# Performance work log

Hardware: AMD Instinct MI355X
Metric: run time of the kernel (lower is better)

## Reference

```python
import jax, jax.numpy as jnp
import numpy as np

EMBED = 512
HEADS = 8
DIM_HEAD = 64
SCALE = DIM_HEAD ** -0.5


def setup_inputs() -> dict:
    key = jax.random.key(0)
    k1, k2, k3 = jax.random.split(key, 3)
    x = jax.random.normal(k1, (1, EMBED, 64, 64), dtype=jnp.float32)
    # nn.Linear(embed, 3*embed) weight [out, in] -> store transposed [in, out] for x @ W
    W_qkv = jax.random.normal(k2, (EMBED, 3 * EMBED), dtype=jnp.float32) * (EMBED ** -0.5)
    b_qkv = jax.random.normal(k3, (3 * EMBED,), dtype=jnp.float32) * 0.01
    return {"x": x, "W_qkv": W_qkv, "b_qkv": b_qkv}


def reference(x, W_qkv, b_qkv):
    B, E, h, w = x.shape
    N = h * w
    # [B, E, H, W] -> [B, N, E]
    xs = x.reshape(B, E, N).transpose(0, 2, 1)
    qkv = xs @ W_qkv + b_qkv                      # [B, N, 3E]
    q, k, v = jnp.split(qkv, 3, axis=-1)          # each [B, N, E]

    def heads(t):
        return t.reshape(B, N, HEADS, DIM_HEAD).transpose(0, 2, 1, 3)  # [B, H, N, dh]

    q, k, v = heads(q), heads(k), heads(v)
    # raw (non-softmax) attention scores, materialized as in the original
    attn = jnp.einsum('bhqd,bhkd->bhqk', q, k) * SCALE  # [B, H, N, N]
    coarse_attn = attn.sum(axis=-2)                     # sum over queries -> [B, H, N]
    output = jnp.einsum('bhqk,bhkd->bhqd', attn, v)     # [B, H, N, dh]
    return coarse_attn, output
```

## Files before the change

kernel.cpp:

```cpp
#include <hip/hip_runtime.h>


#define N_TOK 4096
#define EMBED 512
#define J3    1536
#define HEADS 8
#define DH    64
#define SCALE 0.125f

typedef float  floatx4  __attribute__((ext_vector_type(4)));
typedef short  shortx8  __attribute__((ext_vector_type(8)));
typedef unsigned short ushortx4 __attribute__((ext_vector_type(4)));
typedef unsigned short ushortx2 __attribute__((ext_vector_type(2)));
typedef unsigned int u32;

__device__ inline unsigned short f2bf(float f) {
    union { float f; u32 u; } x; x.f = f;
    u32 r = x.u + 0x7fffu + ((x.u >> 16) & 1u);
    return (unsigned short)(r >> 16);
}
__device__ inline float bf2f(unsigned short u) {
    union { u32 u; float f; } x; x.u = ((u32)u) << 16; return x.f;
}
__device__ static inline void async_copy16(void* lds, const void* g) {
    auto* gp = (const __attribute__((address_space(1))) u32*)g;
    auto* lp = (__attribute__((address_space(3))) u32*)lds;
    __builtin_amdgcn_global_load_lds(gp, lp, 16, 0, 0);
}

__global__ __launch_bounds__(256) void tr_cvt(const float* __restrict__ x,
                                              const float* __restrict__ W,
                                              unsigned short* __restrict__ xT,
                                              unsigned short* __restrict__ WT) {
    const float* src; unsigned short* dst; int C, bx = blockIdx.x;
    if (bx < 64) { src = x; dst = xT; C = N_TOK; }
    else         { src = W; dst = WT; C = J3; bx -= 64; }
    __shared__ float T[64][65];
    const int c0 = bx * 64, r0 = blockIdx.y * 64;
    const int t = threadIdx.x;
    #pragma unroll
    for (int k = 0; k < 16; ++k) {
        int i = t + 256 * k; int r = i >> 6, c = i & 63;
        T[r][c] = src[(size_t)(r0 + r) * C + c0 + c];
    }
    __syncthreads();
    #pragma unroll
    for (int k = 0; k < 4; ++k) {
        int i = t + 256 * k; int cr = i >> 4, cc4 = (i & 15) * 4;
        ushortx4 o = { f2bf(T[cc4 + 0][cr]), f2bf(T[cc4 + 1][cr]),
                       f2bf(T[cc4 + 2][cr]), f2bf(T[cc4 + 3][cr]) };
        *(ushortx4*)&dst[(size_t)(c0 + cr) * 512 + r0 + cc4] = o;
    }
}

__global__ __launch_bounds__(256) void qkv_mfma(const unsigned short* __restrict__ xT,
                                                const unsigned short* __restrict__ WT,
                                                const float* __restrict__ bias,
                                                unsigned short* __restrict__ qkv) {
    __shared__ __align__(16) short As[128 * 32];
    __shared__ __align__(16) short Bs[128 * 32];
    const int j0 = blockIdx.x * 128, n0 = blockIdx.y * 128;
    const int t = threadIdx.x, lane = t & 63, w = t >> 6;
    const int wm = w & 1, wn = w >> 1;
    const int quad = lane >> 4, mrow = lane & 15;
    floatx4 acc[4][4] = {};
    for (int e0 = 0; e0 < 512; e0 += 32) {
        __syncthreads();
        #pragma unroll
        for (int s = 0; s < 2; ++s) {
            int i = t + 256 * s;
            int row = i >> 2, q = i & 3;
            char* abase = (char*)As + (size_t)w * 1024 + (size_t)s * 4096;
            char* bbase = (char*)Bs + (size_t)w * 1024 + (size_t)s * 4096;
            async_copy16(abase, xT + (size_t)(n0 + row) * 512 + e0 + q * 8);
            async_copy16(bbase, WT + (size_t)(j0 + row) * 512 + e0 + q * 8);
        }
        __syncthreads();
        shortx8 a[4], b[4];
        #pragma unroll
        for (int mi = 0; mi < 4; ++mi)
            a[mi] = *(const shortx8*)&As[(wm * 64 + mi * 16 + mrow) * 32 + quad * 8];
        #pragma unroll
        for (int ni = 0; ni < 4; ++ni)
            b[ni] = *(const shortx8*)&Bs[(wn * 64 + ni * 16 + mrow) * 32 + quad * 8];
        #pragma unroll
        for (int mi = 0; mi < 4; ++mi)
            #pragma unroll
            for (int ni = 0; ni < 4; ++ni)
                acc[mi][ni] = __builtin_amdgcn_mfma_f32_16x16x32_bf16(a[mi], b[ni], acc[mi][ni], 0, 0, 0);
    }
    const int col = lane & 15, qr = lane >> 4;
    #pragma unroll
    for (int ni = 0; ni < 4; ++ni) {
        int j = j0 + wn * 64 + ni * 16 + col;
        float bj = bias[j];
        #pragma unroll
        for (int mi = 0; mi < 4; ++mi)
            #pragma unroll
            for (int r = 0; r < 4; ++r) {
                int n = n0 + wm * 64 + mi * 16 + qr * 4 + r;
                qkv[(size_t)n * J3 + j] = f2bf(acc[mi][ni][r] + bj);
            }
    }
}

__global__ __launch_bounds__(256) void kv_partial(const unsigned short* __restrict__ qkv,
                                                  float* __restrict__ Mp, float* __restrict__ qsp) {
    const int h = blockIdx.x, ch = blockIdx.y;
    const int n0 = ch * 64;
    __shared__ __align__(16) float Ks[64][68];
    __shared__ __align__(16) float Vs[64][68];
    __shared__ float qred[256];
    const int t = threadIdx.x;
    #pragma unroll
    for (int k = 0; k < 2; ++k) {
        int i = t + 256 * k; int row = i >> 3, c8 = (i & 7) * 8;
        shortx8 k8 = *(const shortx8*)(qkv + (size_t)(n0 + row) * J3 + EMBED + h * DH + c8);
        shortx8 v8 = *(const shortx8*)(qkv + (size_t)(n0 + row) * J3 + 2 * EMBED + h * DH + c8);
        #pragma unroll
        for (int j = 0; j < 8; ++j) {
            Ks[row][c8 + j] = bf2f((unsigned short)k8[j]);
            Vs[row][c8 + j] = bf2f((unsigned short)v8[j]);
        }
    }
    {
        int d = t & 63, q0 = (t >> 6) * 16;
        float qa = 0.f;
        for (int n = q0; n < q0 + 16; ++n)
            qa += bf2f(qkv[(size_t)(n0 + n) * J3 + h * DH + d]);
        qred[t] = qa;
    }
    __syncthreads();
    const int tx = t & 15, ty = t >> 4;
    float acc[4][4] = {};
    for (int n = 0; n < 64; ++n) {
        floatx4 kf = *(const floatx4*)&Ks[n][ty * 4];
        floatx4 vf = *(const floatx4*)&Vs[n][tx * 4];
        #pragma unroll
        for (int i = 0; i < 4; ++i)
            #pragma unroll
            for (int j = 0; j < 4; ++j)
                acc[i][j] += kf[i] * vf[j];
    }
    float* mp = Mp + ((size_t)h * 64 + ch) * 4096;
    #pragma unroll
    for (int i = 0; i < 4; ++i) {
        floatx4 v = { acc[i][0], acc[i][1], acc[i][2], acc[i][3] };
        *(floatx4*)&mp[(ty * 4 + i) * 64 + tx * 4] = v;
    }
    if (t < 64)
        qsp[((size_t)h * 64 + ch) * 64 + t] = qred[t] + qred[t + 64] + qred[t + 128] + qred[t + 192];
}

__global__ __launch_bounds__(256) void reduce_md(const float* __restrict__ Mp,
                                                 const float* __restrict__ qsp,
                                                 unsigned short* __restrict__ Mt,
                                                 float* __restrict__ qsum) {
    const int h = blockIdx.x, part = blockIdx.y;
    const int t = threadIdx.x;
    __shared__ float Msh[16][68];
    const int i0 = part * 1024 + t * 4;
    floatx4 s = {0.f, 0.f, 0.f, 0.f};
    #pragma unroll 4
    for (int c = 0; c < 64; ++c)
        s += *(const floatx4*)&Mp[((size_t)h * 64 + c) * 4096 + i0];
    const int dpl = t >> 4, d0 = (t & 15) * 4;
    *(floatx4*)&Msh[dpl][d0] = s;
    __syncthreads();
    {
        int d = t >> 2, dpl0 = (t & 3) * 4;
        ushortx4 o = { f2bf(Msh[dpl0 + 0][d]), f2bf(Msh[dpl0 + 1][d]),
                       f2bf(Msh[dpl0 + 2][d]), f2bf(Msh[dpl0 + 3][d]) };
        *(ushortx4*)&Mt[(size_t)h * 4096 + d * 64 + part * 16 + dpl0] = o;
    }
    if (part == 0 && t < 64) {
        float q = 0.f;
        for (int c = 0; c < 64; ++c) q += qsp[((size_t)h * 64 + c) * 64 + t];
        qsum[h * DH + t] = q;
    }
}

__global__ __launch_bounds__(64) void out_kernel(const unsigned short* __restrict__ qkv,
                                                 const unsigned short* __restrict__ Mt,
                                                 const float* __restrict__ qsum,
                                                 float* __restrict__ out) {
    const int h = blockIdx.x, n0 = blockIdx.y * 64;
    const int lane = threadIdx.x;
    const int quad = lane >> 4, mrow = lane & 15;
    floatx4 acc[4][4] = {};
    #pragma unroll
    for (int ks = 0; ks < 2; ++ks) {
        shortx8 a[4], b[4];
        #pragma unroll
        for (int mi = 0; mi < 4; ++mi)
            a[mi] = *(const shortx8*)(qkv + (size_t)(n0 + mi * 16 + mrow) * J3 + h * DH + ks * 32 + quad * 8);
        #pragma unroll
        for (int ni = 0; ni < 4; ++ni)
            b[ni] = *(const shortx8*)(Mt + (size_t)h * 4096 + (ni * 16 + mrow) * 64 + ks * 32 + quad * 8);
        #pragma unroll
        for (int mi = 0; mi < 4; ++mi)
            #pragma unroll
            for (int ni = 0; ni < 4; ++ni)
                acc[mi][ni] = __builtin_amdgcn_mfma_f32_16x16x32_bf16(a[mi], b[ni], acc[mi][ni], 0, 0, 0);
    }
    float* op = out + HEADS * N_TOK + (size_t)h * N_TOK * DH;
    #pragma unroll
    for (int mi = 0; mi < 4; ++mi)
        #pragma unroll
        for (int r = 0; r < 4; ++r) {
            int n = n0 + mi * 16 + quad * 4 + r;
            #pragma unroll
            for (int ni = 0; ni < 4; ++ni)
                op[(size_t)n * DH + ni * 16 + mrow] = acc[mi][ni][r] * SCALE;
        }
    float ca = 0.f;
    #pragma unroll
    for (int g = 0; g < 8; ++g) {
        shortx8 kk = *(const shortx8*)(qkv + (size_t)(n0 + lane) * J3 + EMBED + h * DH + g * 8);
        #pragma unroll
        for (int j = 0; j < 8; ++j)
            ca += bf2f((unsigned short)kk[j]) * qsum[h * DH + g * 8 + j];
    }
    out[h * N_TOK + n0 + lane] = ca * SCALE;
}

extern "C" void kernel_launch(void* const* d_in, const int* in_sizes, int n_in,
                              void* d_out, int out_size, void* d_ws, size_t ws_size,
                              hipStream_t stream) {
    const float* x = (const float*)d_in[0];
    const float* W = (const float*)d_in[1];
    const float* b = (const float*)d_in[2];
    float* out = (float*)d_out;

    unsigned short* xT   = (unsigned short*)d_ws;
    unsigned short* WT   = xT + (size_t)N_TOK * EMBED;
    unsigned short* qkvb = WT + (size_t)J3 * EMBED;
    unsigned short* Mt   = qkvb + (size_t)N_TOK * J3;
    float* Mp   = (float*)(Mt + (size_t)HEADS * DH * DH);
    float* qsp  = Mp + (size_t)HEADS * 64 * 4096;
    float* qsum = qsp + (size_t)HEADS * 64 * 64;

    tr_cvt<<<dim3(88, 8), 256, 0, stream>>>(x, W, xT, WT);
    qkv_mfma<<<dim3(12, 32), 256, 0, stream>>>(xT, WT, b, qkvb);
    kv_partial<<<dim3(8, 64), 256, 0, stream>>>(qkvb, Mp, qsp);
    reduce_md<<<dim3(8, 4), 256, 0, stream>>>(Mp, qsp, Mt, qsum);
    out_kernel<<<dim3(8, 64), 64, 0, stream>>>(qkvb, Mt, qsum, out);
}
```

Baseline: 107.4 us.

## Fold K^T V into weights and compute output via single GEMM from x

Reworks the pipeline algebraically. Q is no longer materialized: the per-head K^T V matrix is folded into the Q weight slice, giving a 640x512 combined matrix. Output and coarse attention are then produced by one GEMM over x. The query column sum is taken from x column sums times W_q plus the bias. K/V projection and the per-chunk K^T V product are fused into one MFMA kernel, so the full qkv buffer is never written. This adds a fold kernel, atomics and a memset, and rounds the folded weights to bf16, which may change accuracy.

```diff
diff --git a/kernel.cpp b/kernel.cpp
--- a/kernel.cpp
+++ b/kernel.cpp
@@ -11,15 +11,15 @@
 typedef float  floatx4  __attribute__((ext_vector_type(4)));
 typedef short  shortx8  __attribute__((ext_vector_type(8)));
 typedef unsigned short ushortx4 __attribute__((ext_vector_type(4)));
-typedef unsigned short ushortx2 __attribute__((ext_vector_type(2)));
 typedef unsigned int u32;
-
-__device__ inline unsigned short f2bf(float f) {
+typedef unsigned short ushort;
+
+__device__ inline ushort f2bf(float f) {
     union { float f; u32 u; } x; x.f = f;
     u32 r = x.u + 0x7fffu + ((x.u >> 16) & 1u);
-    return (unsigned short)(r >> 16);
-}
-__device__ inline float bf2f(unsigned short u) {
+    return (ushort)(r >> 16);
+}
+__device__ inline float bf2f(ushort u) {
     union { u32 u; float f; } x; x.u = ((u32)u) << 16; return x.f;
 }
 __device__ static inline void async_copy16(void* lds, const void* g) {
@@ -28,22 +28,50 @@
     __builtin_amdgcn_global_load_lds(gp, lp, 16, 0, 0);
 }
 
-__global__ __launch_bounds__(256) void tr_cvt(const float* __restrict__ x,
-                                              const float* __restrict__ W,
-                                              unsigned short* __restrict__ xT,
-                                              unsigned short* __restrict__ WT) {
-    const float* src; unsigned short* dst; int C, bx = blockIdx.x;
-    if (bx < 64) { src = x; dst = xT; C = N_TOK; }
-    else         { src = W; dst = WT; C = J3; bx -= 64; }
+__global__ __launch_bounds__(256) void prep(const float* __restrict__ x,
+                                            const float* __restrict__ W,
+                                            ushort* __restrict__ xT,
+                                            ushort* __restrict__ WT,
+                                            ushort* __restrict__ Wb,
+                                            float* __restrict__ xsum) {
+    const int t = threadIdx.x;
+    int bx = blockIdx.x;
+    if (bx >= 88) {
+        if (blockIdx.y != 0) return;
+        const int e0 = (bx - 88) * 32;
+        #pragma unroll
+        for (int k = 0; k < 2; ++k) {
+            int i = t + 256 * k; int row = e0 + (i >> 4), c = (i & 15) * 32;
+            #pragma unroll
+            for (int v = 0; v < 8; ++v) {
+                floatx4 f = *(const floatx4*)(W + (size_t)row * J3 + c + v * 4);
+                ushortx4 o = { f2bf(f[0]), f2bf(f[1]), f2bf(f[2]), f2bf(f[3]) };
+                *(ushortx4*)(Wb + (size_t)row * 512 + c + v * 4) = o;
+            }
+        }
+        return;
+    }
+    const bool isx = bx < 64;
+    const float* src = isx ? x : W;
+    ushort* dst = isx ? xT : WT;
+    const int C = isx ? N_TOK : J3;
+    if (!isx) bx -= 64;
     __shared__ float T[64][65];
+    __shared__ float red[256];
     const int c0 = bx * 64, r0 = blockIdx.y * 64;
-    const int t = threadIdx.x;
     #pragma unroll
     for (int k = 0; k < 16; ++k) {
         int i = t + 256 * k; int r = i >> 6, c = i & 63;
         T[r][c] = src[(size_t)(r0 + r) * C + c0 + c];
     }
     __syncthreads();
+    if (isx) {
+        int row = t >> 2, seg = (t & 3) * 16;
+        float s = 0.f;
+        #pragma unroll
+        for (int cc = 0; cc < 16; ++cc) s += T[row][seg + cc];
+        red[t] = s;
+    }
     #pragma unroll
     for (int k = 0; k < 4; ++k) {
         int i = t + 256 * k; int cr = i >> 4, cc4 = (i & 15) * 4;
@@ -51,114 +79,109 @@
                        f2bf(T[cc4 + 2][cr]), f2bf(T[cc4 + 3][cr]) };
         *(ushortx4*)&dst[(size_t)(c0 + cr) * 512 + r0 + cc4] = o;
     }
-}
-
-__global__ __launch_bounds__(256) void qkv_mfma(const unsigned short* __restrict__ xT,
-                                                const unsigned short* __restrict__ WT,
-                                                const float* __restrict__ bias,
-                                                unsigned short* __restrict__ qkv) {
-    __shared__ __align__(16) short As[128 * 32];
-    __shared__ __align__(16) short Bs[128 * 32];
-    const int j0 = blockIdx.x * 128, n0 = blockIdx.y * 128;
-    const int t = threadIdx.x, lane = t & 63, w = t >> 6;
-    const int wm = w & 1, wn = w >> 1;
-    const int quad = lane >> 4, mrow = lane & 15;
-    floatx4 acc[4][4] = {};
-    for (int e0 = 0; e0 < 512; e0 += 32) {
-        __syncthreads();
-        #pragma unroll
-        for (int s = 0; s < 2; ++s) {
-            int i = t + 256 * s;
-            int row = i >> 2, q = i & 3;
-            char* abase = (char*)As + (size_t)w * 1024 + (size_t)s * 4096;
-            char* bbase = (char*)Bs + (size_t)w * 1024 + (size_t)s * 4096;
-            async_copy16(abase, xT + (size_t)(n0 + row) * 512 + e0 + q * 8);
-            async_copy16(bbase, WT + (size_t)(j0 + row) * 512 + e0 + q * 8);
-        }
-        __syncthreads();
-        shortx8 a[4], b[4];
-        #pragma unroll
-        for (int mi = 0; mi < 4; ++mi)
-            a[mi] = *(const shortx8*)&As[(wm * 64 + mi * 16 + mrow) * 32 + quad * 8];
-        #pragma unroll
-        for (int ni = 0; ni < 4; ++ni)
-            b[ni] = *(const shortx8*)&Bs[(wn * 64 + ni * 16 + mrow) * 32 + quad * 8];
-        #pragma unroll
-        for (int mi = 0; mi < 4; ++mi)
-            #pragma unroll
-            for (int ni = 0; ni < 4; ++ni)
-                acc[mi][ni] = __builtin_amdgcn_mfma_f32_16x16x32_bf16(a[mi], b[ni], acc[mi][ni], 0, 0, 0);
-    }
-    const int col = lane & 15, qr = lane >> 4;
-    #pragma unroll
-    for (int ni = 0; ni < 4; ++ni) {
-        int j = j0 + wn * 64 + ni * 16 + col;
-        float bj = bias[j];
-        #pragma unroll
-        for (int mi = 0; mi < 4; ++mi)
-            #pragma unroll
-            for (int r = 0; r < 4; ++r) {
-                int n = n0 + wm * 64 + mi * 16 + qr * 4 + r;
-                qkv[(size_t)n * J3 + j] = f2bf(acc[mi][ni][r] + bj);
-            }
-    }
-}
-
-__global__ __launch_bounds__(256) void kv_partial(const unsigned short* __restrict__ qkv,
-                                                  float* __restrict__ Mp, float* __restrict__ qsp) {
+    if (isx) {
+        __syncthreads();
+        if ((t & 3) == 0)
+            atomicAdd(&xsum[r0 + (t >> 2)], red[t] + red[t + 1] + red[t + 2] + red[t + 3]);
+    }
+}
+
+__global__ __launch_bounds__(256) void kv_mfma(const ushort* __restrict__ xT,
+                                               const ushort* __restrict__ WT,
+                                               const float* __restrict__ bias,
+                                               float* __restrict__ Mp) {
     const int h = blockIdx.x, ch = blockIdx.y;
     const int n0 = ch * 64;
-    __shared__ __align__(16) float Ks[64][68];
-    __shared__ __align__(16) float Vs[64][68];
-    __shared__ float qred[256];
-    const int t = threadIdx.x;
-    #pragma unroll
-    for (int k = 0; k < 2; ++k) {
-        int i = t + 256 * k; int row = i >> 3, c8 = (i & 7) * 8;
-        shortx8 k8 = *(const shortx8*)(qkv + (size_t)(n0 + row) * J3 + EMBED + h * DH + c8);
-        shortx8 v8 = *(const shortx8*)(qkv + (size_t)(n0 + row) * J3 + 2 * EMBED + h * DH + c8);
-        #pragma unroll
-        for (int j = 0; j < 8; ++j) {
-            Ks[row][c8 + j] = bf2f((unsigned short)k8[j]);
-            Vs[row][c8 + j] = bf2f((unsigned short)v8[j]);
-        }
+    __shared__ __align__(16) short As[64 * 32];
+    __shared__ __align__(16) short Bs[128 * 32];
+    __shared__ __align__(16) short Kt[64 * 72];
+    __shared__ __align__(16) short Vt[64 * 72];
+    const int t = threadIdx.x, lane = t & 63, w = t >> 6;
+    const int quad = lane >> 4, mrow = lane & 15;
+    floatx4 acc[4][2] = {};
+    for (int e0 = 0; e0 < 512; e0 += 32) {
+        __syncthreads();
+        {
+            int row = t >> 2, q = t & 3;
+            async_copy16((char*)As + (size_t)w * 1024,
+                         xT + (size_t)(n0 + row) * 512 + e0 + q * 8);
+        }
+        #pragma unroll
+        for (int s = 0; s < 2; ++s) {
+            int i = t + 256 * s; int row = i >> 2, q = i & 3;
+            int j = (row < 64) ? (512 + h * 64 + row) : (1024 + h * 64 + row - 64);
+            async_copy16((char*)Bs + (size_t)w * 1024 + (size_t)s * 4096,
+                         WT + (size_t)j * 512 + e0 + q * 8);
+        }
+        __syncthreads();
+        shortx8 a[4], b[2];
+        #pragma unroll
+        for (int mi = 0; mi < 4; ++mi)
+            a[mi] = *(const shortx8*)&As[(mi * 16 + mrow) * 32 + quad * 8];
+        #pragma unroll
+        for (int ni = 0; ni < 2; ++ni)
+            b[ni] = *(const shortx8*)&Bs[(w * 32 + ni * 16 + mrow) * 32 + quad * 8];
+        #pragma unroll
+        for (int mi = 0; mi < 4; ++mi)
+            #pragma unroll
+            for (int ni = 0; ni < 2; ++ni)
+                acc[mi][ni] = __builtin_amdgcn_mfma_f32_16x16x32_bf16(a[mi], b[ni], acc[mi][ni], 0, 0, 0);
     }
     {
-        int d = t & 63, q0 = (t >> 6) * 16;
-        float qa = 0.f;
-        for (int n = q0; n < q0 + 16; ++n)
-            qa += bf2f(qkv[(size_t)(n0 + n) * J3 + h * DH + d]);
-        qred[t] = qa;
+        short* dst = (w < 2) ? Kt : Vt;
+        const int dhb = (w & 1) * 32;
+        const int boff = (w < 2) ? 512 : 1024;
+        #pragma unroll
+        for (int ni = 0; ni < 2; ++ni) {
+            int dh = dhb + ni * 16 + (lane & 15);
+            float bj = bias[boff + h * 64 + dh];
+            #pragma unroll
+            for (int mi = 0; mi < 4; ++mi)
+                #pragma unroll
+                for (int r = 0; r < 4; ++r) {
+                    int tok = mi * 16 + quad * 4 + r;
+                    dst[dh * 72 + tok] = (short)f2bf(acc[mi][ni][r] + bj);
+                }
+        }
     }
     __syncthreads();
-    const int tx = t & 15, ty = t >> 4;
-    float acc[4][4] = {};
-    for (int n = 0; n < 64; ++n) {
-        floatx4 kf = *(const floatx4*)&Ks[n][ty * 4];
-        floatx4 vf = *(const floatx4*)&Vs[n][tx * 4];
-        #pragma unroll
-        for (int i = 0; i < 4; ++i)
-            #pragma unroll
-            for (int j = 0; j < 4; ++j)
-                acc[i][j] += kf[i] * vf[j];
+    const int dpb = (w & 1) * 32, db = (w >> 1) * 32;
+    floatx4 m[2][2] = {};
+    #pragma unroll
+    for (int kt = 0; kt < 2; ++kt) {
+        shortx8 ka[2], vb[2];
+        #pragma unroll
+        for (int fi = 0; fi < 2; ++fi)
+            ka[fi] = *(const shortx8*)&Kt[(dpb + fi * 16 + mrow) * 72 + kt * 32 + quad * 8];
+        #pragma unroll
+        for (int fj = 0; fj < 2; ++fj)
+            vb[fj] = *(const shortx8*)&Vt[(db + fj * 16 + mrow) * 72 + kt * 32 + quad * 8];
+        #pragma unroll
+        for (int fi = 0; fi < 2; ++fi)
+            #pragma unroll
+            for (int fj = 0; fj < 2; ++fj)
+                m[fi][fj] = __builtin_amdgcn_mfma_f32_16x16x32_bf16(ka[fi], vb[fj], m[fi][fj], 0, 0, 0);
     }
     float* mp = Mp + ((size_t)h * 64 + ch) * 4096;
     #pragma unroll
-    for (int i = 0; i < 4; ++i) {
-        floatx4 v = { acc[i][0], acc[i][1], acc[i][2], acc[i][3] };
-        *(floatx4*)&mp[(ty * 4 + i) * 64 + tx * 4] = v;
-    }
-    if (t < 64)
-        qsp[((size_t)h * 64 + ch) * 64 + t] = qred[t] + qred[t + 64] + qred[t + 128] + qred[t + 192];
-}
-
-__global__ __launch_bounds__(256) void reduce_md(const float* __restrict__ Mp,
-                                                 const float* __restrict__ qsp,
-                                                 unsigned short* __restrict__ Mt,
+    for (int fi = 0; fi < 2; ++fi)
+        #pragma unroll
+        for (int fj = 0; fj < 2; ++fj)
+            #pragma unroll
+            for (int r = 0; r < 4; ++r)
+                mp[(dpb + fi * 16 + quad * 4 + r) * 64 + db + fj * 16 + (lane & 15)] = m[fi][fj][r];
+}
+
+__global__ __launch_bounds__(256) void reduce_qm(const float* __restrict__ Mp,
+                                                 const ushort* __restrict__ WT,
+                                                 const float* __restrict__ bias,
+                                                 const float* __restrict__ xsum,
+                                                 ushort* __restrict__ Mt,
                                                  float* __restrict__ qsum) {
     const int h = blockIdx.x, part = blockIdx.y;
     const int t = threadIdx.x;
     __shared__ float Msh[16][68];
+    __shared__ float red[256];
     const int i0 = part * 1024 + t * 4;
     floatx4 s = {0.f, 0.f, 0.f, 0.f};
     #pragma unroll 4
@@ -173,55 +196,143 @@
                        f2bf(Msh[dpl0 + 2][d]), f2bf(Msh[dpl0 + 3][d]) };
         *(ushortx4*)&Mt[(size_t)h * 4096 + d * 64 + part * 16 + dpl0] = o;
     }
-    if (part == 0 && t < 64) {
-        float q = 0.f;
-        for (int c = 0; c < 64; ++c) q += qsp[((size_t)h * 64 + c) * 64 + t];
-        qsum[h * DH + t] = q;
-    }
-}
-
-__global__ __launch_bounds__(64) void out_kernel(const unsigned short* __restrict__ qkv,
-                                                 const unsigned short* __restrict__ Mt,
-                                                 const float* __restrict__ qsum,
-                                                 float* __restrict__ out) {
-    const int h = blockIdx.x, n0 = blockIdx.y * 64;
-    const int lane = threadIdx.x;
+    {
+        int row = t >> 4, seg = (t & 15) * 32;
+        int j = h * 64 + part * 16 + row;
+        float qa = 0.f;
+        #pragma unroll
+        for (int g = 0; g < 4; ++g) {
+            shortx8 wv = *(const shortx8*)(WT + (size_t)j * 512 + seg + g * 8);
+            #pragma unroll
+            for (int u = 0; u < 8; ++u)
+                qa += bf2f((ushort)wv[u]) * xsum[seg + g * 8 + u];
+        }
+        red[t] = qa;
+    }
+    __syncthreads();
+    if (t < 16) {
+        float tot = 0.f;
+        #pragma unroll
+        for (int g = 0; g < 16; ++g) tot += red[t * 16 + g];
+        int j = h * 64 + part * 16 + t;
+        qsum[j] = 4096.f * bias[j] + tot;
+    }
+}
+
+__global__ __launch_bounds__(256) void fold(const ushort* __restrict__ Wb,
+                                            const float* __restrict__ W,
+                                            const float* __restrict__ bias,
+                                            const ushort* __restrict__ Mt,
+                                            const float* __restrict__ qsum,
+                                            ushort* __restrict__ B2,
+                                            float* __restrict__ b2) {
+    const int h = blockIdx.x;
+    const int t = threadIdx.x, lane = t & 63, w = t >> 6;
+    const int quad = lane >> 4, mrow = lane & 15;
+    for (int pos = w; pos < 128; pos += 4) {
+        int mi = pos >> 5, nj = pos & 31;
+        floatx4 d4 = {};
+        #pragma unroll
+        for (int k = 0; k < 2; ++k) {
+            shortx8 a = *(const shortx8*)(Mt + (size_t)h * 4096 + (mi * 16 + mrow) * 64 + k * 32 + quad * 8);
+            shortx8 b = *(const shortx8*)(Wb + (size_t)(nj * 16 + mrow) * 512 + h * 64 + k * 32 + quad * 8);
+            d4 = __builtin_amdgcn_mfma_f32_16x16x32_bf16(a, b, d4, 0, 0, 0);
+        }
+        #pragma unroll
+        for (int r = 0; r < 4; ++r) {
+            int d = mi * 16 + quad * 4 + r, e = nj * 16 + (lane & 15);
+            B2[(size_t)(h * 64 + d) * 512 + e] = f2bf(d4[r]);
+        }
+    }
+    for (int e = t; e < 512; e += 256) {
+        const float* wr = W + (size_t)e * J3 + 512 + h * 64;
+        const float* qh = qsum + h * 64;
+        float s = 0.f;
+        #pragma unroll 8
+        for (int dp = 0; dp < 64; ++dp) s += wr[dp] * qh[dp];
+        B2[(size_t)(512 + h) * 512 + e] = f2bf(s);
+    }
+    {
+        shortx8 z = {};
+        for (int idx = t; idx < 960; idx += 256)
+            *(shortx8*)(B2 + (size_t)(520 + h * 15) * 512 + idx * 8) = z;
+    }
+    if (t < 64) {
+        float s = 0.f;
+        #pragma unroll 8
+        for (int dp = 0; dp < 64; ++dp)
+            s += bias[h * 64 + dp] * bf2f(Mt[(size_t)h * 4096 + t * 64 + dp]);
+        b2[h * 64 + t] = s;
+    } else if (t == 64) {
+        float s = 0.f;
+        for (int dp = 0; dp < 64; ++dp)
+            s += bias[512 + h * 64 + dp] * qsum[h * 64 + dp];
+        b2[512 + h] = s;
+    }
+    if (h == 0 && t >= 128 && t < 248) b2[520 + (t - 128)] = 0.f;
+}
+
+__global__ __launch_bounds__(256) void out_gemm(const ushort* __restrict__ xT,
+                                                const ushort* __restrict__ B2,
+                                                const float* __restrict__ b2,
+                                                float* __restrict__ out) {
+    __shared__ __align__(16) short As[128 * 32];
+    __shared__ __align__(16) short Bs[128 * 32];
+    const int j0 = blockIdx.x * 128, n0 = blockIdx.y * 128;
+    const int t = threadIdx.x, lane = t & 63, w = t >> 6;
+    const int wm = w & 1, wn = w >> 1;
     const int quad = lane >> 4, mrow = lane & 15;
     floatx4 acc[4][4] = {};
-    #pragma unroll
-    for (int ks = 0; ks < 2; ++ks) {
+    for (int e0 = 0; e0 < 512; e0 += 32) {
+        __syncthreads();
+        #pragma unroll
+        for (int s = 0; s < 2; ++s) {
+            int i = t + 256 * s; int row = i >> 2, q = i & 3;
+            async_copy16((char*)As + (size_t)w * 1024 + (size_t)s * 4096,
+                         xT + (size_t)(n0 + row) * 512 + e0 + q * 8);
+            async_copy16((char*)Bs + (size_t)w * 1024 + (size_t)s * 4096,
+                         B2 + (size_t)(j0 + row) * 512 + e0 + q * 8);
+        }
+        __syncthreads();
         shortx8 a[4], b[4];
         #pragma unroll
         for (int mi = 0; mi < 4; ++mi)
-            a[mi] = *(const shortx8*)(qkv + (size_t)(n0 + mi * 16 + mrow) * J3 + h * DH + ks * 32 + quad * 8);
+            a[mi] = *(const shortx8*)&As[(wm * 64 + mi * 16 + mrow) * 32 + quad * 8];
         #pragma unroll
         for (int ni = 0; ni < 4; ++ni)
-            b[ni] = *(const shortx8*)(Mt + (size_t)h * 4096 + (ni * 16 + mrow) * 64 + ks * 32 + quad * 8);
+            b[ni] = *(const shortx8*)&Bs[(wn * 64 + ni * 16 + mrow) * 32 + quad * 8];
         #pragma unroll
         for (int mi = 0; mi < 4; ++mi)
             #pragma unroll
             for (int ni = 0; ni < 4; ++ni)
                 acc[mi][ni] = __builtin_amdgcn_mfma_f32_16x16x32_bf16(a[mi], b[ni], acc[mi][ni], 0, 0, 0);
     }
-    float* op = out + HEADS * N_TOK + (size_t)h * N_TOK * DH;
-    #pragma unroll
-    for (int mi = 0; mi < 4; ++mi)
-        #pragma unroll
-        for (int r = 0; r < 4; ++r) {
-            int n = n0 + mi * 16 + quad * 4 + r;
-            #pragma unroll
-            for (int ni = 0; ni < 4; ++ni)
-                op[(size_t)n * DH + ni * 16 + mrow] = acc[mi][ni][r] * SCALE;
-        }
-    float ca = 0.f;
-    #pragma unroll
-    for (int g = 0; g < 8; ++g) {
-        shortx8 kk = *(const shortx8*)(qkv + (size_t)(n0 + lane) * J3 + EMBED + h * DH + g * 8);
-        #pragma unroll
-        for (int j = 0; j < 8; ++j)
-            ca += bf2f((unsigned short)kk[j]) * qsum[h * DH + g * 8 + j];
-    }
-    out[h * N_TOK + n0 + lane] = ca * SCALE;
+    const int col = lane & 15, qr = lane >> 4;
+    #pragma unroll
+    for (int ni = 0; ni < 4; ++ni) {
+        int j = j0 + wn * 64 + ni * 16 + col;
+        float bj = b2[j];
+        if (j < 512) {
+            int hh = j >> 6, d = j & 63;
+            float* op = out + HEADS * N_TOK + (size_t)hh * N_TOK * DH + d;
+            #pragma unroll
+            for (int mi = 0; mi < 4; ++mi)
+                #pragma unroll
+                for (int r = 0; r < 4; ++r) {
+                    int n = n0 + wm * 64 + mi * 16 + qr * 4 + r;
+                    op[(size_t)n * DH] = SCALE * (acc[mi][ni][r] + bj);
+                }
+        } else if (j < 520) {
+            int hh = j - 512;
+            #pragma unroll
+            for (int mi = 0; mi < 4; ++mi)
+                #pragma unroll
+                for (int r = 0; r < 4; ++r) {
+                    int n = n0 + wm * 64 + mi * 16 + qr * 4 + r;
+                    out[hh * N_TOK + n] = SCALE * (acc[mi][ni][r] + bj);
+                }
+        }
+    }
 }
 
 extern "C" void kernel_launch(void* const* d_in, const int* in_sizes, int n_in,
@@ -232,17 +343,20 @@
     const float* b = (const float*)d_in[2];
     float* out = (float*)d_out;
 
-    unsigned short* xT   = (unsigned short*)d_ws;
-    unsigned short* WT   = xT + (size_t)N_TOK * EMBED;
-    unsigned short* qkvb = WT + (size_t)J3 * EMBED;
-    unsigned short* Mt   = qkvb + (size_t)N_TOK * J3;
-    float* Mp   = (float*)(Mt + (size_t)HEADS * DH * DH);
-    float* qsp  = Mp + (size_t)HEADS * 64 * 4096;
-    float* qsum = qsp + (size_t)HEADS * 64 * 64;
-
-    tr_cvt<<<dim3(88, 8), 256, 0, stream>>>(x, W, xT, WT);
-    qkv_mfma<<<dim3(12, 32), 256, 0, stream>>>(xT, WT, b, qkvb);
-    kv_partial<<<dim3(8, 64), 256, 0, stream>>>(qkvb, Mp, qsp);
-    reduce_md<<<dim3(8, 4), 256, 0, stream>>>(Mp, qsp, Mt, qsum);
-    out_kernel<<<dim3(8, 64), 64, 0, stream>>>(qkvb, Mt, qsum, out);
-}
+    ushort* xT = (ushort*)d_ws;
+    ushort* WT = xT + (size_t)N_TOK * EMBED;
+    ushort* Wb = WT + (size_t)J3 * EMBED;
+    ushort* Mt = Wb + (size_t)EMBED * EMBED;
+    ushort* B2 = Mt + (size_t)HEADS * DH * DH;
+    float* Mp   = (float*)(B2 + (size_t)640 * 512);
+    float* xsum = Mp + (size_t)HEADS * 64 * 4096;
+    float* qsum = xsum + 512;
+    float* b2   = qsum + 512;
+
+    hipMemsetAsync(xsum, 0, 512 * sizeof(float), stream);
+    prep<<<dim3(104, 8), 256, 0, stream>>>(x, W, xT, WT, Wb, xsum);
+    kv_mfma<<<dim3(8, 64), 256, 0, stream>>>(xT, WT, b, Mp);
+    reduce_qm<<<dim3(8, 4), 256, 0, stream>>>(Mp, WT, b, xsum, Mt, qsum);
+    fold<<<8, 256, 0, stream>>>(Wb, W, b, Mt, qsum, B2, b2);
+    out_gemm<<<dim3(5, 32), 256, 0, stream>>>(xT, B2, b2, out);
+}
```

After: 127.5 us. +18.7%, slower.
